# Kernel optimization log

Hardware: AMD Instinct MI355X
Metric: run time of the kernel (lower is better)

## Reference

```python
import jax, jax.numpy as jnp
import numpy as np

IN_FEATURES = 4096
OUT_FEATURES = 4096
NNZ = 838860
BATCH = 512


def setup_inputs() -> dict:
    key = jax.random.key(0)
    kx, kr, kc, kv, kb = jax.random.split(key, 5)
    x = jax.random.normal(kx, (BATCH, IN_FEATURES), dtype=jnp.float32)
    row_idx = jax.random.randint(kr, (NNZ,), 0, OUT_FEATURES, dtype=jnp.int64)
    col_idx = jax.random.randint(kc, (NNZ,), 0, IN_FEATURES, dtype=jnp.int64)
    values = jax.random.normal(kv, (NNZ,), dtype=jnp.float32)
    bias = jax.random.normal(kb, (OUT_FEATURES,), dtype=jnp.float32)
    return {"x": x, "row_idx": row_idx, "col_idx": col_idx,
            "values": values, "bias": bias}


def reference(x, row_idx, col_idx, values, bias):
    # COO sparse linear: y[b, row] += x[b, col] * val, then add bias.
    x_flat = x.reshape(-1, IN_FEATURES)                    # [B, in]
    weighted = x_flat[:, col_idx] * values                 # [B, nnz]
    out = jnp.zeros((x_flat.shape[0], OUT_FEATURES), dtype=x.dtype)
    out = out.at[:, row_idx].add(weighted)                 # scatter-add per row
    out = out + bias
    return out.reshape(x.shape[:-1] + (OUT_FEATURES,))
```

## Files before the change

### kernel.cpp

```cpp
#include <hip/hip_runtime.h>

#define IN_F    4096
#define OUT_F   4096
#define K_DIM   4096
#define NNZ_C   838860
#define NQ      (NNZ_C / 4)
#define BATCH   512
#define BK      32
#define BM      128
#define BN      128

typedef short bf16x8 __attribute__((ext_vector_type(8)));
typedef float f32x4  __attribute__((ext_vector_type(4)));
typedef unsigned int u32x4 __attribute__((ext_vector_type(4)));

__device__ __forceinline__ unsigned short f2bf(float f) {
    unsigned u = __float_as_uint(f);
    u += 0x7fffu + ((u >> 16) & 1u);
    return (unsigned short)(u >> 16);
}
__device__ __forceinline__ void gload_lds16(const void* g, void* l) {
    __builtin_amdgcn_global_load_lds(
        (const __attribute__((address_space(1))) unsigned int*)g,
        (__attribute__((address_space(3))) unsigned int*)l, 16, 0, 0);
}
__device__ __forceinline__ void pk_add(unsigned short* W, unsigned idx, float v) {
    unsigned short h = f2bf(v);
    unsigned data = (idx & 1u) ? ((unsigned)h << 16) : (unsigned)h;
    unsigned long long addr = (unsigned long long)(W + (idx & ~1u));
    asm volatile("global_atomic_pk_add_bf16 %0, %1, off"
                 :: "v"(addr), "v"(data) : "memory");
}

#define N_WZ   (OUT_F * K_DIM / 8)
#define N_CVT  (BATCH * K_DIM / 8)
#define N_OUT  (BATCH * OUT_F / 4)
__global__ void prep(const float* __restrict__ x,
                     unsigned short* __restrict__ xb,
                     const float* __restrict__ bias,
                     float* __restrict__ out,
                     u32x4* __restrict__ Wz, int do_bias) {
    int i = blockIdx.x * 256 + threadIdx.x;
    if (i < N_WZ) {
        __builtin_nontemporal_store((u32x4){0u, 0u, 0u, 0u}, &Wz[i]);
        return;
    }
    i -= N_WZ;
    if (i < N_CVT) {
        const float4* p = (const float4*)x + (size_t)i * 2;
        float4 a = p[0], b = p[1];
        union { unsigned short h[8]; bf16x8 v; } u;
        u.h[0] = f2bf(a.x); u.h[1] = f2bf(a.y); u.h[2] = f2bf(a.z); u.h[3] = f2bf(a.w);
        u.h[4] = f2bf(b.x); u.h[5] = f2bf(b.y); u.h[6] = f2bf(b.z); u.h[7] = f2bf(b.w);
        ((bf16x8*)xb)[i] = u.v;
        return;
    }
    i -= N_CVT;
    if (i < N_OUT && do_bias) {
        float4 b = ((const float4*)bias)[i & (OUT_F / 4 - 1)];
        ((float4*)out)[i] = b;
    }
}
#define PREP_BLOCKS ((N_WZ + N_CVT + N_OUT) / 256)

__global__ void scatter_pk(const int* __restrict__ row_idx,
                           const int* __restrict__ col_idx,
                           const float* __restrict__ values,
                           unsigned short* __restrict__ W) {
    int i = blockIdx.x * 256 + threadIdx.x;
    if (i >= NQ) return;
    int4   r4 = ((const int4*)row_idx)[i];
    int4   c4 = ((const int4*)col_idx)[i];
    float4 v4 = ((const float4*)values)[i];
    pk_add(W, (unsigned)r4.x * K_DIM + (unsigned)c4.x, v4.x);
    pk_add(W, (unsigned)r4.y * K_DIM + (unsigned)c4.y, v4.y);
    pk_add(W, (unsigned)r4.z * K_DIM + (unsigned)c4.z, v4.z);
    pk_add(W, (unsigned)r4.w * K_DIM + (unsigned)c4.w, v4.w);
}

template <int EPI, int SK>
__global__ void __launch_bounds__(256)
gemm_bt(const unsigned short* __restrict__ Abf,
        const unsigned short* __restrict__ Wbf,
        const float* __restrict__ bias,
        float* __restrict__ out,
        float* __restrict__ parts) {
    __shared__ __align__(16) unsigned short As[BM * BK];
    __shared__ __align__(16) unsigned short Bs[BN * BK];

    const int nt = blockIdx.x, mt = blockIdx.y, s = blockIdx.z;
    const int t = threadIdx.x, w = t >> 6, ln = t & 63;
    const int wm = w & 1, wn = w >> 1;
    const int KSs = K_DIM / SK;
    const int ks0 = s * KSs;

    const int srow = w * 16 + (ln >> 2);
    const int scol = (((ln & 3) ^ ((ln >> 3) & 3)) * 8);
    const unsigned short* gA0 = Abf + (size_t)(mt * BM + srow) * K_DIM + ks0 + scol;
    const unsigned short* gA1 = gA0 + (size_t)64 * K_DIM;
    const unsigned short* gB0 = Wbf + (size_t)(nt * BN + srow) * K_DIM + ks0 + scol;
    const unsigned short* gB1 = gB0 + (size_t)64 * K_DIM;
    unsigned short* lA0 = &As[(w * 16) * BK];
    unsigned short* lA1 = &As[(64 + w * 16) * BK];
    unsigned short* lB0 = &Bs[(w * 16) * BK];
    unsigned short* lB1 = &Bs[(64 + w * 16) * BK];

    const int quad = ln >> 4, lanem = ln & 15;
    const int rsw = (quad ^ ((lanem >> 1) & 3)) * 8;
    const unsigned short* rA = &As[(wm * 64 + lanem) * BK + rsw];
    const unsigned short* rB = &Bs[(wn * 64 + lanem) * BK + rsw];

    f32x4 acc[4][4];
#pragma unroll
    for (int mi = 0; mi < 4; ++mi)
#pragma unroll
        for (int ni = 0; ni < 4; ++ni)
            acc[mi][ni] = (f32x4){0.f, 0.f, 0.f, 0.f};

    for (int kt = 0; kt < KSs / BK; ++kt) {
        __syncthreads();
        gload_lds16(gA0 + kt * BK, lA0);
        gload_lds16(gA1 + kt * BK, lA1);
        gload_lds16(gB0 + kt * BK, lB0);
        gload_lds16(gB1 + kt * BK, lB1);
        __syncthreads();

        bf16x8 af[4], bfr[4];
#pragma unroll
        for (int mi = 0; mi < 4; ++mi) af[mi]  = *(const bf16x8*)(rA + mi * 16 * BK);
#pragma unroll
        for (int ni = 0; ni < 4; ++ni) bfr[ni] = *(const bf16x8*)(rB + ni * 16 * BK);
#pragma unroll
        for (int mi = 0; mi < 4; ++mi)
#pragma unroll
            for (int ni = 0; ni < 4; ++ni)
                acc[mi][ni] = __builtin_amdgcn_mfma_f32_16x16x32_bf16(
                    af[mi], bfr[ni], acc[mi][ni], 0, 0, 0);
    }

    const int row0 = mt * BM + wm * 64 + quad * 4;
    const int col0 = nt * BN + wn * 64 + lanem;
    if (EPI == 0) {
        if (s == 0) {
            float bv[4];
#pragma unroll
            for (int ni = 0; ni < 4; ++ni) bv[ni] = bias[col0 + ni * 16];
#pragma unroll
            for (int mi = 0; mi < 4; ++mi)
#pragma unroll
                for (int ni = 0; ni < 4; ++ni)
#pragma unroll
                    for (int r = 0; r < 4; ++r)
                        out[(size_t)(row0 + mi * 16 + r) * OUT_F + col0 + ni * 16] =
                            acc[mi][ni][r] + bv[ni];
        } else {
            float* dst = parts + (size_t)(s - 1) * BATCH * OUT_F;
#pragma unroll
            for (int mi = 0; mi < 4; ++mi)
#pragma unroll
                for (int ni = 0; ni < 4; ++ni)
#pragma unroll
                    for (int r = 0; r < 4; ++r)
                        __builtin_nontemporal_store(
                            acc[mi][ni][r],
                            &dst[(size_t)(row0 + mi * 16 + r) * OUT_F + col0 + ni * 16]);
        }
    } else {
#pragma unroll
        for (int mi = 0; mi < 4; ++mi)
#pragma unroll
            for (int ni = 0; ni < 4; ++ni)
#pragma unroll
                for (int r = 0; r < 4; ++r)
                    atomicAdd(&out[(size_t)(row0 + mi * 16 + r) * OUT_F + col0 + ni * 16],
                              acc[mi][ni][r]);
    }
}

__global__ void reduce_parts(float* __restrict__ out,
                             const float* __restrict__ parts) {
    int i = blockIdx.x * 256 + threadIdx.x;
    float4 a = ((const float4*)out)[i];
#pragma unroll
    for (int p = 0; p < 7; ++p) {
        float4 b = ((const float4*)(parts + (size_t)p * BATCH * OUT_F))[i];
        a.x += b.x; a.y += b.y; a.z += b.z; a.w += b.w;
    }
    ((float4*)out)[i] = a;
}

extern "C" void kernel_launch(void* const* d_in, const int* in_sizes, int n_in,
                              void* d_out, int out_size, void* d_ws, size_t ws_size,
                              hipStream_t stream) {
    const float* x       = (const float*)d_in[0];
    const int*   row_idx = (const int*)d_in[1];
    const int*   col_idx = (const int*)d_in[2];
    const float* values  = (const float*)d_in[3];
    const float* bias    = (const float*)d_in[4];
    float*       out     = (float*)d_out;

    unsigned short* xb = (unsigned short*)d_ws;
    unsigned short* W  = xb + (size_t)BATCH * K_DIM;
    float* parts = (float*)(W + (size_t)OUT_F * K_DIM);
    size_t need = (size_t)BATCH * K_DIM * 2 + (size_t)OUT_F * K_DIM * 2
                + (size_t)7 * BATCH * OUT_F * 4;
    bool use_parts = (ws_size >= need);

    prep<<<PREP_BLOCKS, 256, 0, stream>>>(x, xb, bias, out, (u32x4*)W,
                                          use_parts ? 0 : 1);
    scatter_pk<<<(NQ + 255) / 256, 256, 0, stream>>>(
        row_idx, col_idx, values, W);

    if (use_parts) {
        gemm_bt<0, 8><<<dim3(OUT_F / BN, BATCH / BM, 8), 256, 0, stream>>>(
            xb, W, bias, out, parts);
        reduce_parts<<<BATCH * OUT_F / 4 / 256, 256, 0, stream>>>(out, parts);
    } else {
        gemm_bt<1, 4><<<dim3(OUT_F / BN, BATCH / BM, 4), 256, 0, stream>>>(
            xb, W, bias, out, nullptr);
    }
}
```

Before: 175.2 us.

## Fuse scatter and split-K GEMM into one persistent kernel with per-chunk flags

```diff
diff --git a/kernel.cpp b/kernel.cpp
--- a/kernel.cpp
+++ b/kernel.cpp
@@ -9,10 +9,11 @@
 #define BK      32
 #define BM      128
 #define BN      128
+#define NBLK    1024
+#define NCHUNK  8
 
 typedef short bf16x8 __attribute__((ext_vector_type(8)));
 typedef float f32x4  __attribute__((ext_vector_type(4)));
-typedef unsigned int u32x4 __attribute__((ext_vector_type(4)));
 
 __device__ __forceinline__ unsigned short f2bf(float f) {
     unsigned u = __float_as_uint(f);
@@ -30,6 +31,176 @@
     unsigned long long addr = (unsigned long long)(W + (idx & ~1u));
     asm volatile("global_atomic_pk_add_bf16 %0, %1, off"
                  :: "v"(addr), "v"(data) : "memory");
+}
+
+template <int EPI, int SK>
+__device__ __forceinline__ void gemm_body(
+    int nt, int mt, int s, int t,
+    const unsigned short* __restrict__ Abf,
+    const unsigned short* __restrict__ Wbf,
+    const float* __restrict__ bias,
+    float* __restrict__ out, float* __restrict__ parts,
+    unsigned short* As, unsigned short* Bs) {
+    const int w = t >> 6, ln = t & 63;
+    const int wm = w & 1, wn = w >> 1;
+    const int KSs = K_DIM / SK;
+    const int ks0 = s * KSs;
+
+    const int srow = w * 16 + (ln >> 2);
+    const int scol = (((ln & 3) ^ ((ln >> 3) & 3)) * 8);
+    const unsigned short* gA0 = Abf + (size_t)(mt * BM + srow) * K_DIM + ks0 + scol;
+    const unsigned short* gA1 = gA0 + (size_t)64 * K_DIM;
+    const unsigned short* gB0 = Wbf + (size_t)(nt * BN + srow) * K_DIM + ks0 + scol;
+    const unsigned short* gB1 = gB0 + (size_t)64 * K_DIM;
+    unsigned short* lA0 = &As[(w * 16) * BK];
+    unsigned short* lA1 = &As[(64 + w * 16) * BK];
+    unsigned short* lB0 = &Bs[(w * 16) * BK];
+    unsigned short* lB1 = &Bs[(64 + w * 16) * BK];
+
+    const int quad = ln >> 4, lanem = ln & 15;
+    const int rsw = (quad ^ ((lanem >> 1) & 3)) * 8;
+    const unsigned short* rA = &As[(wm * 64 + lanem) * BK + rsw];
+    const unsigned short* rB = &Bs[(wn * 64 + lanem) * BK + rsw];
+
+    f32x4 acc[4][4];
+#pragma unroll
+    for (int mi = 0; mi < 4; ++mi)
+#pragma unroll
+        for (int ni = 0; ni < 4; ++ni)
+            acc[mi][ni] = (f32x4){0.f, 0.f, 0.f, 0.f};
+
+    for (int kt = 0; kt < KSs / BK; ++kt) {
+        __syncthreads();
+        gload_lds16(gA0 + kt * BK, lA0);
+        gload_lds16(gA1 + kt * BK, lA1);
+        gload_lds16(gB0 + kt * BK, lB0);
+        gload_lds16(gB1 + kt * BK, lB1);
+        __syncthreads();
+
+        bf16x8 af[4], bfr[4];
+#pragma unroll
+        for (int mi = 0; mi < 4; ++mi) af[mi]  = *(const bf16x8*)(rA + mi * 16 * BK);
+#pragma unroll
+        for (int ni = 0; ni < 4; ++ni) bfr[ni] = *(const bf16x8*)(rB + ni * 16 * BK);
+#pragma unroll
+        for (int mi = 0; mi < 4; ++mi)
+#pragma unroll
+            for (int ni = 0; ni < 4; ++ni)
+                acc[mi][ni] = __builtin_amdgcn_mfma_f32_16x16x32_bf16(
+                    af[mi], bfr[ni], acc[mi][ni], 0, 0, 0);
+    }
+
+    const int row0 = mt * BM + wm * 64 + quad * 4;
+    const int col0 = nt * BN + wn * 64 + lanem;
+    if (EPI == 0) {
+        if (s == 0) {
+            float bv[4];
+#pragma unroll
+            for (int ni = 0; ni < 4; ++ni) bv[ni] = bias[col0 + ni * 16];
+#pragma unroll
+            for (int mi = 0; mi < 4; ++mi)
+#pragma unroll
+                for (int ni = 0; ni < 4; ++ni)
+#pragma unroll
+                    for (int r = 0; r < 4; ++r)
+                        out[(size_t)(row0 + mi * 16 + r) * OUT_F + col0 + ni * 16] =
+                            acc[mi][ni][r] + bv[ni];
+        } else {
+            float* dst = parts + (size_t)(s - 1) * BATCH * OUT_F;
+#pragma unroll
+            for (int mi = 0; mi < 4; ++mi)
+#pragma unroll
+                for (int ni = 0; ni < 4; ++ni)
+#pragma unroll
+                    for (int r = 0; r < 4; ++r)
+                        dst[(size_t)(row0 + mi * 16 + r) * OUT_F + col0 + ni * 16] =
+                            acc[mi][ni][r];
+        }
+    } else {
+#pragma unroll
+        for (int mi = 0; mi < 4; ++mi)
+#pragma unroll
+            for (int ni = 0; ni < 4; ++ni)
+#pragma unroll
+                for (int r = 0; r < 4; ++r)
+                    atomicAdd(&out[(size_t)(row0 + mi * 16 + r) * OUT_F + col0 + ni * 16],
+                              acc[mi][ni][r]);
+    }
+}
+
+__global__ void cvt_x(const float* __restrict__ x,
+                      unsigned short* __restrict__ xb) {
+    int i = blockIdx.x * 256 + threadIdx.x;
+    const float4* p = (const float4*)x + (size_t)i * 2;
+    float4 a = p[0], b = p[1];
+    union { unsigned short h[8]; bf16x8 v; } u;
+    u.h[0] = f2bf(a.x); u.h[1] = f2bf(a.y); u.h[2] = f2bf(a.z); u.h[3] = f2bf(a.w);
+    u.h[4] = f2bf(b.x); u.h[5] = f2bf(b.y); u.h[6] = f2bf(b.z); u.h[7] = f2bf(b.w);
+    ((bf16x8*)xb)[i] = u.v;
+}
+
+__global__ void __launch_bounds__(256, 4)
+scatter_gemm(const int* __restrict__ row_idx,
+             const int* __restrict__ col_idx,
+             const float* __restrict__ values,
+             const unsigned short* __restrict__ xb,
+             unsigned short* __restrict__ W,
+             const float* __restrict__ bias,
+             float* __restrict__ out,
+             float* __restrict__ parts,
+             int* __restrict__ done) {
+    __shared__ __align__(16) unsigned short As[BM * BK];
+    __shared__ __align__(16) unsigned short Bs[BN * BK];
+    const int b = blockIdx.x, t = threadIdx.x;
+    const int g = b * 256 + t;
+
+    unsigned eidx[4];
+    float    ev[4];
+    const bool have = (g < NQ);
+    if (have) {
+        int4   r4 = ((const int4*)row_idx)[g];
+        int4   c4 = ((const int4*)col_idx)[g];
+        float4 v4 = ((const float4*)values)[g];
+        eidx[0] = (unsigned)r4.x * K_DIM + (unsigned)c4.x;  ev[0] = v4.x;
+        eidx[1] = (unsigned)r4.y * K_DIM + (unsigned)c4.y;  ev[1] = v4.y;
+        eidx[2] = (unsigned)r4.z * K_DIM + (unsigned)c4.z;  ev[2] = v4.z;
+        eidx[3] = (unsigned)r4.w * K_DIM + (unsigned)c4.w;  ev[3] = v4.w;
+    }
+
+    for (int c = 0; c < NCHUNK; ++c) {
+        if (have) {
+#pragma unroll
+            for (int j = 0; j < 4; ++j)
+                if ((int)((eidx[j] >> 9) & 7u) == c) pk_add(W, eidx[j], ev[j]);
+        }
+        asm volatile("s_waitcnt vmcnt(0)" ::: "memory");
+        __syncthreads();
+        if (t == 0)
+            __hip_atomic_fetch_add(&done[c * 32], 1,
+                                   __ATOMIC_RELEASE, __HIP_MEMORY_SCOPE_AGENT);
+    }
+
+    const int s = b >> 7, nt = b & 31, mt = (b >> 5) & 3;
+    if (t == 0) {
+        while (__hip_atomic_load(&done[s * 32], __ATOMIC_ACQUIRE,
+                                 __HIP_MEMORY_SCOPE_AGENT) < NBLK)
+            __builtin_amdgcn_s_sleep(8);
+    }
+    __syncthreads();
+
+    gemm_body<0, 8>(nt, mt, s, t, xb, W, bias, out, parts, As, Bs);
+}
+
+__global__ void reduce_parts(float* __restrict__ out,
+                             const float* __restrict__ parts) {
+    int i = blockIdx.x * 256 + threadIdx.x;
+    float4 a = ((const float4*)out)[i];
+#pragma unroll
+    for (int p = 0; p < 7; ++p) {
+        float4 b = ((const float4*)(parts + (size_t)p * BATCH * OUT_F))[i];
+        a.x += b.x; a.y += b.y; a.z += b.z; a.w += b.w;
+    }
+    ((float4*)out)[i] = a;
 }
 
 #define N_WZ   (OUT_F * K_DIM / 8)
@@ -39,12 +210,9 @@
                      unsigned short* __restrict__ xb,
                      const float* __restrict__ bias,
                      float* __restrict__ out,
-                     u32x4* __restrict__ Wz, int do_bias) {
+                     uint4* __restrict__ Wz, int do_bias) {
     int i = blockIdx.x * 256 + threadIdx.x;
-    if (i < N_WZ) {
-        __builtin_nontemporal_store((u32x4){0u, 0u, 0u, 0u}, &Wz[i]);
-        return;
-    }
+    if (i < N_WZ) { Wz[i] = make_uint4(0, 0, 0, 0); return; }
     i -= N_WZ;
     if (i < N_CVT) {
         const float4* p = (const float4*)x + (size_t)i * 2;
@@ -61,8 +229,6 @@
         ((float4*)out)[i] = b;
     }
 }
-#define PREP_BLOCKS ((N_WZ + N_CVT + N_OUT) / 256)
-
 __global__ void scatter_pk(const int* __restrict__ row_idx,
                            const int* __restrict__ col_idx,
                            const float* __restrict__ values,
@@ -77,116 +243,19 @@
     pk_add(W, (unsigned)r4.z * K_DIM + (unsigned)c4.z, v4.z);
     pk_add(W, (unsigned)r4.w * K_DIM + (unsigned)c4.w, v4.w);
 }
-
-template <int EPI, int SK>
 __global__ void __launch_bounds__(256)
-gemm_bt(const unsigned short* __restrict__ Abf,
-        const unsigned short* __restrict__ Wbf,
-        const float* __restrict__ bias,
-        float* __restrict__ out,
-        float* __restrict__ parts) {
+gemm_k(const unsigned short* __restrict__ Abf,
+       const unsigned short* __restrict__ Wbf,
+       const float* __restrict__ bias,
+       float* __restrict__ out, float* __restrict__ parts, int epi) {
     __shared__ __align__(16) unsigned short As[BM * BK];
     __shared__ __align__(16) unsigned short Bs[BN * BK];
-
-    const int nt = blockIdx.x, mt = blockIdx.y, s = blockIdx.z;
-    const int t = threadIdx.x, w = t >> 6, ln = t & 63;
-    const int wm = w & 1, wn = w >> 1;
-    const int KSs = K_DIM / SK;
-    const int ks0 = s * KSs;
-
-    const int srow = w * 16 + (ln >> 2);
-    const int scol = (((ln & 3) ^ ((ln >> 3) & 3)) * 8);
-    const unsigned short* gA0 = Abf + (size_t)(mt * BM + srow) * K_DIM + ks0 + scol;
-    const unsigned short* gA1 = gA0 + (size_t)64 * K_DIM;
-    const unsigned short* gB0 = Wbf + (size_t)(nt * BN + srow) * K_DIM + ks0 + scol;
-    const unsigned short* gB1 = gB0 + (size_t)64 * K_DIM;
-    unsigned short* lA0 = &As[(w * 16) * BK];
-    unsigned short* lA1 = &As[(64 + w * 16) * BK];
-    unsigned short* lB0 = &Bs[(w * 16) * BK];
-    unsigned short* lB1 = &Bs[(64 + w * 16) * BK];
-
-    const int quad = ln >> 4, lanem = ln & 15;
-    const int rsw = (quad ^ ((lanem >> 1) & 3)) * 8;
-    const unsigned short* rA = &As[(wm * 64 + lanem) * BK + rsw];
-    const unsigned short* rB = &Bs[(wn * 64 + lanem) * BK + rsw];
-
-    f32x4 acc[4][4];
-#pragma unroll
-    for (int mi = 0; mi < 4; ++mi)
-#pragma unroll
-        for (int ni = 0; ni < 4; ++ni)
-            acc[mi][ni] = (f32x4){0.f, 0.f, 0.f, 0.f};
-
-    for (int kt = 0; kt < KSs / BK; ++kt) {
-        __syncthreads();
-        gload_lds16(gA0 + kt * BK, lA0);
-        gload_lds16(gA1 + kt * BK, lA1);
-        gload_lds16(gB0 + kt * BK, lB0);
-        gload_lds16(gB1 + kt * BK, lB1);
-        __syncthreads();
-
-        bf16x8 af[4], bfr[4];
-#pragma unroll
-        for (int mi = 0; mi < 4; ++mi) af[mi]  = *(const bf16x8*)(rA + mi * 16 * BK);
-#pragma unroll
-        for (int ni = 0; ni < 4; ++ni) bfr[ni] = *(const bf16x8*)(rB + ni * 16 * BK);
-#pragma unroll
-        for (int mi = 0; mi < 4; ++mi)
-#pragma unroll
-            for (int ni = 0; ni < 4; ++ni)
-                acc[mi][ni] = __builtin_amdgcn_mfma_f32_16x16x32_bf16(
-                    af[mi], bfr[ni], acc[mi][ni], 0, 0, 0);
-    }
-
-    const int row0 = mt * BM + wm * 64 + quad * 4;
-    const int col0 = nt * BN + wn * 64 + lanem;
-    if (EPI == 0) {
-        if (s == 0) {
-            float bv[4];
-#pragma unroll
-            for (int ni = 0; ni < 4; ++ni) bv[ni] = bias[col0 + ni * 16];
-#pragma unroll
-            for (int mi = 0; mi < 4; ++mi)
-#pragma unroll
-                for (int ni = 0; ni < 4; ++ni)
-#pragma unroll
-                    for (int r = 0; r < 4; ++r)
-                        out[(size_t)(row0 + mi * 16 + r) * OUT_F + col0 + ni * 16] =
-                            acc[mi][ni][r] + bv[ni];
-        } else {
-            float* dst = parts + (size_t)(s - 1) * BATCH * OUT_F;
-#pragma unroll
-            for (int mi = 0; mi < 4; ++mi)
-#pragma unroll
-                for (int ni = 0; ni < 4; ++ni)
-#pragma unroll
-                    for (int r = 0; r < 4; ++r)
-                        __builtin_nontemporal_store(
-                            acc[mi][ni][r],
-                            &dst[(size_t)(row0 + mi * 16 + r) * OUT_F + col0 + ni * 16]);
-        }
-    } else {
-#pragma unroll
-        for (int mi = 0; mi < 4; ++mi)
-#pragma unroll
-            for (int ni = 0; ni < 4; ++ni)
-#pragma unroll
-                for (int r = 0; r < 4; ++r)
-                    atomicAdd(&out[(size_t)(row0 + mi * 16 + r) * OUT_F + col0 + ni * 16],
-                              acc[mi][ni][r]);
-    }
-}
-
-__global__ void reduce_parts(float* __restrict__ out,
-                             const float* __restrict__ parts) {
-    int i = blockIdx.x * 256 + threadIdx.x;
-    float4 a = ((const float4*)out)[i];
-#pragma unroll
-    for (int p = 0; p < 7; ++p) {
-        float4 b = ((const float4*)(parts + (size_t)p * BATCH * OUT_F))[i];
-        a.x += b.x; a.y += b.y; a.z += b.z; a.w += b.w;
-    }
-    ((float4*)out)[i] = a;
+    if (epi == 0)
+        gemm_body<0, 8>(blockIdx.x, blockIdx.y, blockIdx.z, threadIdx.x,
+                        Abf, Wbf, bias, out, parts, As, Bs);
+    else
+        gemm_body<1, 4>(blockIdx.x, blockIdx.y, blockIdx.z, threadIdx.x,
+                        Abf, Wbf, bias, out, parts, As, Bs);
 }
 
 extern "C" void kernel_launch(void* const* d_in, const int* in_sizes, int n_in,
@@ -199,24 +268,39 @@
     const float* bias    = (const float*)d_in[4];
     float*       out     = (float*)d_out;
 
-    unsigned short* xb = (unsigned short*)d_ws;
-    unsigned short* W  = xb + (size_t)BATCH * K_DIM;
-    float* parts = (float*)(W + (size_t)OUT_F * K_DIM);
-    size_t need = (size_t)BATCH * K_DIM * 2 + (size_t)OUT_F * K_DIM * 2
-                + (size_t)7 * BATCH * OUT_F * 4;
-    bool use_parts = (ws_size >= need);
-
-    prep<<<PREP_BLOCKS, 256, 0, stream>>>(x, xb, bias, out, (u32x4*)W,
-                                          use_parts ? 0 : 1);
-    scatter_pk<<<(NQ + 255) / 256, 256, 0, stream>>>(
-        row_idx, col_idx, values, W);
-
-    if (use_parts) {
-        gemm_bt<0, 8><<<dim3(OUT_F / BN, BATCH / BM, 8), 256, 0, stream>>>(
-            xb, W, bias, out, parts);
+    char* p = (char*)d_ws;
+    unsigned short* xb = (unsigned short*)p; p += (size_t)BATCH * K_DIM * 2;
+    unsigned short* W  = (unsigned short*)p; p += (size_t)OUT_F * K_DIM * 2;
+    int* done = (int*)p;                     p += 4096;
+    float* parts = (float*)p;                p += (size_t)7 * BATCH * OUT_F * 4;
+    size_t need_full = (size_t)(p - (char*)d_ws);
+    size_t need_parts = need_full;
+
+    int maxb = 0;
+    hipError_t e = hipOccupancyMaxActiveBlocksPerMultiprocessor(
+        &maxb, (const void*)scatter_gemm, 256, 0);
+    bool fuse = (e == hipSuccess) && (maxb >= 4) && (ws_size >= need_full);
+
+    if (fuse) {
+        hipMemsetAsync(W, 0, (size_t)OUT_F * K_DIM * 2 + 4096, stream);
+        cvt_x<<<NBLK, 256, 0, stream>>>(x, xb);
+        scatter_gemm<<<NBLK, 256, 0, stream>>>(row_idx, col_idx, values,
+                                               xb, W, bias, out, parts, done);
+        reduce_parts<<<BATCH * OUT_F / 4 / 256, 256, 0, stream>>>(out, parts);
+    } else if (ws_size >= need_parts) {
+        prep<<<(N_WZ + N_CVT + N_OUT) / 256, 256, 0, stream>>>(
+            x, xb, bias, out, (uint4*)W, 0);
+        scatter_pk<<<(NQ + 255) / 256, 256, 0, stream>>>(
+            row_idx, col_idx, values, W);
+        gemm_k<<<dim3(OUT_F / BN, BATCH / BM, 8), 256, 0, stream>>>(
+            xb, W, bias, out, parts, 0);
         reduce_parts<<<BATCH * OUT_F / 4 / 256, 256, 0, stream>>>(out, parts);
     } else {
-        gemm_bt<1, 4><<<dim3(OUT_F / BN, BATCH / BM, 4), 256, 0, stream>>>(
-            xb, W, bias, out, nullptr);
-    }
-}
+        prep<<<(N_WZ + N_CVT + N_OUT) / 256, 256, 0, stream>>>(
+            x, xb, bias, out, (uint4*)W, 1);
+        scatter_pk<<<(NQ + 255) / 256, 256, 0, stream>>>(
+            row_idx, col_idx, values, W);
+        gemm_k<<<dim3(OUT_F / BN, BATCH / BM, 4), 256, 0, stream>>>(
+            xb, W, bias, out, nullptr, 1);
+    }
+}
```

Measured after the change: 164.8 us. -5.9%, faster.
